# Kernel optimization log

Measured on AMD Instinct MI355X. Metric: run time of the kernel, lower is better.

Reference implementation:

```python
import jax, jax.numpy as jnp
import numpy as np

GLOW_SIZE = 51
GLOW_SIGMA = 15.0


def _glow_kernel():
    # 1D gaussian, normalized, then outer product -> dense 51x51 kernel (as in torch module)
    grid = jnp.arange(GLOW_SIZE, dtype=jnp.float32) - GLOW_SIZE // 2
    g = jnp.exp(-grid ** 2 / (2.0 * GLOW_SIGMA * GLOW_SIGMA))
    g = g / g.sum()
    k2d = jnp.outer(g, g)  # [51, 51]
    # depthwise kernel OIHW with feature_group_count=3: [3, 1, 51, 51]
    return jnp.broadcast_to(k2d, (3, 1, GLOW_SIZE, GLOW_SIZE))


def setup_inputs() -> dict:
    key = jax.random.key(0)
    kx, = jax.random.split(key, 1)
    x = jax.random.uniform(kx, (8, 3, 1024, 1024), dtype=jnp.float32)  # images in [0,1]
    amount_param = jnp.zeros((), dtype=jnp.float32)  # nn.Parameter(torch.tensor(0.0))
    return {"x": x, "amount_param": amount_param}


def reference(x, amount_param):
    amount = jax.nn.sigmoid(amount_param) * 0.4  # 0.2 at init, so no early return
    kernel = _glow_kernel()
    pad = GLOW_SIZE // 2
    # per-channel (depthwise) 51x51 gaussian blur, same padding
    glow = jax.lax.conv_general_dilated(
        x, kernel,
        window_strides=(1, 1),
        padding=[(pad, pad), (pad, pad)],
        dimension_numbers=("NCHW", "OIHW", "NCHW"),
        feature_group_count=3,
    )
    glow = glow * 1.2
    # screen blend + clamp
    result = 1.0 - (1.0 - x) * (1.0 - glow * amount)
    return jnp.clip(result, 0.0, 1.0)
```

## Files before the change

### kernel.cpp

```cpp
#include <hip/hip_runtime.h>
#include <cmath>

#define HH 1024
#define WW 1024
#define KS 51
#define RAD 25
#define PLANE (HH * WW)

struct GaussW { float w[KS]; };

__global__ __launch_bounds__(256) void hblur_kernel(const float* __restrict__ x,
                                                    float* __restrict__ tmp,
                                                    GaussW gw)
{
    __shared__ __align__(16) float lds[4][1024];

    const int t    = threadIdx.x;
    const int lane = t & 63;
    const int r    = t >> 6;
    const long long row = (long long)blockIdx.x * 4 + r;
    const float* src = x + row * WW;
    char* Lrow = (char*)&lds[r][0];

    #define SWZ(b) ((b) ^ ((((b) >> 7) & 7) << 4))

    #pragma unroll
    for (int g = 0; g < 4; g++) {
        const int c = g * 256 + lane * 4;
        float4 v = *(const float4*)(src + c);
        *(float4*)(Lrow + SWZ(c * 4)) = v;
    }

    const int j0 = lane * 16;
    float acc[16];
    #pragma unroll
    for (int d = 0; d < 16; d++) acc[d] = 0.f;

    #pragma unroll
    for (int i = 0; i < 18; i++) {
        const int col = j0 - 28 + i * 4;
        const bool in = ((unsigned)col < (unsigned)WW);
        const int cc = in ? col : 0;
        float4 vv = *(const float4*)(Lrow + SWZ(cc * 4));
        if (!in) vv = make_float4(0.f, 0.f, 0.f, 0.f);
        const float vq[4] = {vv.x, vv.y, vv.z, vv.w};
        #pragma unroll
        for (int q = 0; q < 4; q++) {
            const int wi = i * 4 + q;
            #pragma unroll
            for (int d = 0; d < 16; d++) {
                const int k = wi - 3 - d;
                if (k >= 0 && k < KS)
                    acc[d] = fmaf(gw.w[k], vq[q], acc[d]);
            }
        }
    }

    #pragma unroll
    for (int g = 0; g < 4; g++) {
        const int c = j0 + g * 4;
        *(float4*)(Lrow + SWZ(c * 4)) =
            make_float4(acc[g*4], acc[g*4+1], acc[g*4+2], acc[g*4+3]);
    }

    float* dst = tmp + row * WW;
    #pragma unroll
    for (int g = 0; g < 4; g++) {
        const int c = g * 256 + lane * 4;
        float4 v = *(const float4*)(Lrow + SWZ(c * 4));
        *(float4*)(dst + c) = v;
    }
    #undef SWZ
}

__global__ __launch_bounds__(256) void vblend_kernel(const float* __restrict__ tmp,
                                                     const float* __restrict__ x,
                                                     float* __restrict__ out,
                                                     GaussW gw,
                                                     const float* __restrict__ amountp)
{
    __shared__ __align__(16) float s[114 * 128];

    const int t      = threadIdx.x;
    const int bid    = blockIdx.x;
    const int plane  = bid >> 7;
    const int rem    = bid & 127;
    const int tile_x = rem >> 4;
    const int tile_y = rem & 15;
    const int cb     = tile_x * 128;
    const int rb     = tile_y * 64;

    const float* tpl = tmp + (size_t)plane * PLANE;

    #pragma unroll
    for (int it = 0; it < 15; it++) {
        const int idx = it * 256 + t;
        if (idx < 114 * 32) {
            const int row = idx >> 5;
            const int c4  = idx & 31;
            const int gr  = rb - 25 + row;
            const int grc = min(max(gr, 0), HH - 1);
            float4 v = *(const float4*)(tpl + (size_t)grc * WW + cb + c4 * 4);
            if ((unsigned)gr >= (unsigned)HH) v = make_float4(0.f, 0.f, 0.f, 0.f);
            *(float4*)(&s[row * 128 + c4 * 4]) = v;
        }
    }
    __syncthreads();

    const int lane = t & 63;
    const int wid  = t >> 6;
    const int lr0  = wid * 16;
    const int c0l  = lane * 2;

    float2 acc[16];
    #pragma unroll
    for (int j = 0; j < 16; j++) acc[j] = make_float2(0.f, 0.f);

    #pragma unroll
    for (int i = 0; i < 66; i++) {
        const float2 v = *(const float2*)(&s[(lr0 + i) * 128 + c0l]);
        #pragma unroll
        for (int j = 0; j < 16; j++) {
            const int k = i - j;
            if (k >= 0 && k < KS) {
                const float wk = gw.w[k];
                acc[j].x = fmaf(wk, v.x, acc[j].x);
                acc[j].y = fmaf(wk, v.y, acc[j].y);
            }
        }
    }

    const float p = amountp[0];
    const float sc = 1.2f * (0.4f / (1.f + expf(-p)));

    const int r0 = rb + lr0;
    const int c0 = cb + c0l;
    const float* xp = x   + (size_t)plane * PLANE + c0;
    float*       op = out + (size_t)plane * PLANE + c0;
    #pragma unroll
    for (int j = 0; j < 16; j++) {
        const float2 xv = *(const float2*)(xp + (size_t)(r0 + j) * WW);
        float2 res;
        res.x = 1.f - (1.f - xv.x) * (1.f - sc * acc[j].x);
        res.y = 1.f - (1.f - xv.y) * (1.f - sc * acc[j].y);
        res.x = fminf(fmaxf(res.x, 0.f), 1.f);
        res.y = fminf(fmaxf(res.y, 0.f), 1.f);
        *(float2*)(op + (size_t)(r0 + j) * WW) = res;
    }
}

extern "C" void kernel_launch(void* const* d_in, const int* in_sizes, int n_in,
                              void* d_out, int out_size, void* d_ws, size_t ws_size,
                              hipStream_t stream)
{
    const float* x       = (const float*)d_in[0];
    const float* amountp = (const float*)d_in[1];
    float* out = (float*)d_out;
    float* tmp = (float*)d_ws;

    GaussW gw;
    {
        double e[KS], sum = 0.0;
        for (int i = 0; i < KS; i++) {
            const double d = (double)(i - RAD);
            e[i] = exp(-d * d / (2.0 * 15.0 * 15.0));
            sum += e[i];
        }
        for (int i = 0; i < KS; i++) gw.w[i] = (float)(e[i] / sum);
    }

    const int total_planes = in_sizes[0] / PLANE;
    const size_t plane_bytes = (size_t)PLANE * sizeof(float);
    int P = (int)(ws_size / plane_bytes);
    if (P < 1) P = 1;
    if (P > total_planes) P = total_planes;

    for (int p0 = 0; p0 < total_planes; p0 += P) {
        const int pc = (total_planes - p0 < P) ? (total_planes - p0) : P;
        hblur_kernel<<<pc * 256, 256, 0, stream>>>(x + (size_t)p0 * PLANE, tmp, gw);
        vblend_kernel<<<pc * 128, 256, 0, stream>>>(tmp,
                                                    x + (size_t)p0 * PLANE,
                                                    out + (size_t)p0 * PLANE,
                                                    gw, amountp);
    }
}
```

Measured before the change: 236.5 us.

## Narrow vertical-blur tiles to 64 columns and preload horizontal-blur LDS reads

The vertical blend kernel now processes 64-column tiles with one column per lane instead of 128 columns with two per lane. This halves LDS per block and the accumulator registers, and doubles the block count to raise occupancy and parallelism. It costs more redundant halo rows loaded per output and narrower scalar global accesses. The horizontal blur kernel now loads all 18 float4 LDS values into registers before the FMA loop, separating loads from compute at the cost of higher register pressure.

```diff
diff --git a/kernel.cpp b/kernel.cpp
--- a/kernel.cpp
+++ b/kernel.cpp
@@ -32,10 +32,8 @@
     }
 
     const int j0 = lane * 16;
-    float acc[16];
-    #pragma unroll
-    for (int d = 0; d < 16; d++) acc[d] = 0.f;
 
+    float4 v[18];
     #pragma unroll
     for (int i = 0; i < 18; i++) {
         const int col = j0 - 28 + i * 4;
@@ -43,7 +41,16 @@
         const int cc = in ? col : 0;
         float4 vv = *(const float4*)(Lrow + SWZ(cc * 4));
         if (!in) vv = make_float4(0.f, 0.f, 0.f, 0.f);
-        const float vq[4] = {vv.x, vv.y, vv.z, vv.w};
+        v[i] = vv;
+    }
+
+    float acc[16];
+    #pragma unroll
+    for (int d = 0; d < 16; d++) acc[d] = 0.f;
+
+    #pragma unroll
+    for (int i = 0; i < 18; i++) {
+        const float vq[4] = {v[i].x, v[i].y, v[i].z, v[i].w};
         #pragma unroll
         for (int q = 0; q < 4; q++) {
             const int wi = i * 4 + q;
@@ -67,8 +74,8 @@
     #pragma unroll
     for (int g = 0; g < 4; g++) {
         const int c = g * 256 + lane * 4;
-        float4 v = *(const float4*)(Lrow + SWZ(c * 4));
-        *(float4*)(dst + c) = v;
+        float4 vv = *(const float4*)(Lrow + SWZ(c * 4));
+        *(float4*)(dst + c) = vv;
     }
     #undef SWZ
 }
@@ -79,30 +86,30 @@
                                                      GaussW gw,
                                                      const float* __restrict__ amountp)
 {
-    __shared__ __align__(16) float s[114 * 128];
+    __shared__ __align__(16) float s[114 * 64];
 
     const int t      = threadIdx.x;
     const int bid    = blockIdx.x;
-    const int plane  = bid >> 7;
-    const int rem    = bid & 127;
+    const int plane  = bid >> 8;
+    const int rem    = bid & 255;
     const int tile_x = rem >> 4;
     const int tile_y = rem & 15;
-    const int cb     = tile_x * 128;
+    const int cb     = tile_x * 64;
     const int rb     = tile_y * 64;
 
     const float* tpl = tmp + (size_t)plane * PLANE;
 
     #pragma unroll
-    for (int it = 0; it < 15; it++) {
+    for (int it = 0; it < 8; it++) {
         const int idx = it * 256 + t;
-        if (idx < 114 * 32) {
-            const int row = idx >> 5;
-            const int c4  = idx & 31;
+        if (idx < 114 * 16) {
+            const int row = idx >> 4;
+            const int c4  = idx & 15;
             const int gr  = rb - 25 + row;
             const int grc = min(max(gr, 0), HH - 1);
             float4 v = *(const float4*)(tpl + (size_t)grc * WW + cb + c4 * 4);
             if ((unsigned)gr >= (unsigned)HH) v = make_float4(0.f, 0.f, 0.f, 0.f);
-            *(float4*)(&s[row * 128 + c4 * 4]) = v;
+            *(float4*)(&s[row * 64 + c4 * 4]) = v;
         }
     }
     __syncthreads();
@@ -110,23 +117,19 @@
     const int lane = t & 63;
     const int wid  = t >> 6;
     const int lr0  = wid * 16;
-    const int c0l  = lane * 2;
 
-    float2 acc[16];
+    float acc[16];
     #pragma unroll
-    for (int j = 0; j < 16; j++) acc[j] = make_float2(0.f, 0.f);
+    for (int j = 0; j < 16; j++) acc[j] = 0.f;
 
     #pragma unroll
     for (int i = 0; i < 66; i++) {
-        const float2 v = *(const float2*)(&s[(lr0 + i) * 128 + c0l]);
+        const float v = s[(lr0 + i) * 64 + lane];
         #pragma unroll
         for (int j = 0; j < 16; j++) {
             const int k = i - j;
-            if (k >= 0 && k < KS) {
-                const float wk = gw.w[k];
-                acc[j].x = fmaf(wk, v.x, acc[j].x);
-                acc[j].y = fmaf(wk, v.y, acc[j].y);
-            }
+            if (k >= 0 && k < KS)
+                acc[j] = fmaf(gw.w[k], v, acc[j]);
         }
     }
 
@@ -134,18 +137,15 @@
     const float sc = 1.2f * (0.4f / (1.f + expf(-p)));
 
     const int r0 = rb + lr0;
-    const int c0 = cb + c0l;
+    const int c0 = cb + lane;
     const float* xp = x   + (size_t)plane * PLANE + c0;
     float*       op = out + (size_t)plane * PLANE + c0;
     #pragma unroll
     for (int j = 0; j < 16; j++) {
-        const float2 xv = *(const float2*)(xp + (size_t)(r0 + j) * WW);
-        float2 res;
-        res.x = 1.f - (1.f - xv.x) * (1.f - sc * acc[j].x);
-        res.y = 1.f - (1.f - xv.y) * (1.f - sc * acc[j].y);
-        res.x = fminf(fmaxf(res.x, 0.f), 1.f);
-        res.y = fminf(fmaxf(res.y, 0.f), 1.f);
-        *(float2*)(op + (size_t)(r0 + j) * WW) = res;
+        const float xv = xp[(size_t)(r0 + j) * WW];
+        float res = 1.f - (1.f - xv) * (1.f - sc * acc[j]);
+        res = fminf(fmaxf(res, 0.f), 1.f);
+        op[(size_t)(r0 + j) * WW] = res;
     }
 }
 
@@ -178,7 +178,7 @@
     for (int p0 = 0; p0 < total_planes; p0 += P) {
         const int pc = (total_planes - p0 < P) ? (total_planes - p0) : P;
         hblur_kernel<<<pc * 256, 256, 0, stream>>>(x + (size_t)p0 * PLANE, tmp, gw);
-        vblend_kernel<<<pc * 128, 256, 0, stream>>>(tmp,
+        vblend_kernel<<<pc * 256, 256, 0, stream>>>(tmp,
                                                     x + (size_t)p0 * PLANE,
                                                     out + (size_t)p0 * PLANE,
                                                     gw, amountp);
```

New measurement: 239.4 us. About the same (+1.2%).
